# Kernel tuning notes

Hardware: AMD Instinct MI355X
Metric: run time of the kernel (lower is better)

## Reference

```python
import jax, jax.numpy as jnp
import numpy as np

N_NODES = 100000
N_EDGES = 3200000
HID = 16


def _graph_conv(x, src, dst, w_rel, w_root, b_rel, num_nodes):
    # PyG GraphConv: out_i = lin_rel(sum_{j in N(i)} x_j) + lin_root(x_i)
    agg = jax.ops.segment_sum(x[src], dst, num_segments=num_nodes)  # [N, d_in]
    return agg @ w_rel + b_rel + x @ w_root


def setup_inputs() -> dict:
    key = jax.random.key(0)
    ks = jax.random.split(key, 8)
    x = jax.random.normal(ks[0], (N_NODES, 1), dtype=jnp.float32)
    edge_index = jax.random.randint(ks[1], (2, N_EDGES), 0, N_NODES, dtype=jnp.int64)
    s = 1.0 / np.sqrt(HID)
    return {
        "x": x,
        "edge_index": edge_index,
        "enc_w_rel": jax.random.uniform(ks[2], (1, HID), jnp.float32, -1.0, 1.0),
        "enc_w_root": jax.random.uniform(ks[3], (1, HID), jnp.float32, -1.0, 1.0),
        "enc_b": jnp.zeros((HID,), jnp.float32),
        "proc_w_rel": jax.random.uniform(ks[4], (HID, HID), jnp.float32, -s, s),
        "proc_w_root": jax.random.uniform(ks[5], (HID, HID), jnp.float32, -s, s),
        "proc_b": jnp.zeros((HID,), jnp.float32),
        "dec_w_rel": jax.random.uniform(ks[6], (HID, 1), jnp.float32, -s, s),
        "dec_w_root": jax.random.uniform(ks[7], (HID, 1), jnp.float32, -s, s),
        "dec_b": jnp.zeros((1,), jnp.float32),
    }


def reference(x, edge_index, enc_w_rel, enc_w_root, enc_b,
              proc_w_rel, proc_w_root, proc_b,
              dec_w_rel, dec_w_root, dec_b):
    num_nodes = x.shape[0]
    src, dst = edge_index[0], edge_index[1]
    z = _graph_conv(x, src, dst, enc_w_rel, enc_w_root, enc_b, num_nodes)
    z = jax.nn.relu(z)
    z = _graph_conv(z, src, dst, proc_w_rel, proc_w_root, proc_b, num_nodes)
    y = _graph_conv(z, src, dst, dec_w_rel, dec_w_root, dec_b, num_nodes)
    return jax.nn.relu(y)
```

## Files before the change

kernel.cpp:

```cpp
#include <hip/hip_runtime.h>
#include <hip/hip_bf16.h>

#define HID 16
#define SB_BITS 11
#define SBLK (1 << SB_BITS)
#define SUBS 128
#define NBMAX 64
#define GSTRIDE 16
#define PT_THREADS 256
#define PT_K 16
#define PT_EDGES (PT_THREADS * PT_K)
#define ROWP 65

__global__ void k_init(int* __restrict__ p, int n) {
    int i = blockIdx.x * blockDim.x + threadIdx.x;
    if (i < n) p[i] = 0;
}

__global__ void k_passA(const int* __restrict__ src, const int* __restrict__ dst,
                        unsigned* __restrict__ bucketsA, int* __restrict__ gcurA,
                        int E, int nb, int capA) {
    __shared__ int cnt[NBMAX];
    __shared__ int pos[NBMAX];
    __shared__ int gbase[NBMAX];
    __shared__ unsigned reorder[PT_EDGES];
    __shared__ unsigned char bbk[PT_EDGES];
    int tb = blockIdx.x * PT_EDGES;
    int nE = min(PT_EDGES, E - tb);
    if (threadIdx.x < nb) cnt[threadIdx.x] = 0;
    __syncthreads();
    int kk[PT_K]; int rk[PT_K]; unsigned pk[PT_K];
#pragma unroll
    for (int k = 0; k < PT_K; k++) {
        int e = tb + k * PT_THREADS + threadIdx.x;
        if (e < E) {
            int s = src[e], d = dst[e];
            int b = d >> SB_BITS;
            kk[k] = b;
            pk[k] = ((unsigned)(d & (SBLK - 1)) << 17) | (unsigned)s;
            rk[k] = atomicAdd(&cnt[b], 1);
        } else kk[k] = -1;
    }
    __syncthreads();
    if (threadIdx.x == 0) {
        int acc = 0;
        for (int b = 0; b < nb; b++) { pos[b] = acc; acc += cnt[b]; }
    }
    __syncthreads();
    if (threadIdx.x < nb && cnt[threadIdx.x] > 0)
        gbase[threadIdx.x] = atomicAdd(&gcurA[threadIdx.x * GSTRIDE], cnt[threadIdx.x]);
    __syncthreads();
#pragma unroll
    for (int k = 0; k < PT_K; k++) {
        if (kk[k] >= 0) {
            int idx = pos[kk[k]] + rk[k];
            reorder[idx] = pk[k];
            bbk[idx] = (unsigned char)kk[k];
        }
    }
    __syncthreads();
    for (int idx = threadIdx.x; idx < nE; idx += PT_THREADS) {
        int b = bbk[idx];
        int g = gbase[b] + (idx - pos[b]);
        if (g < capA) bucketsA[(size_t)b * capA + g] = reorder[idx];
    }
}

__global__ void k_passB(const unsigned* __restrict__ bucketsA, const int* __restrict__ gcurA,
                        unsigned* __restrict__ bucketsB, int* __restrict__ gcurB,
                        int capA, int capSub, int tilesB) {
    int j = blockIdx.x / tilesB;
    int tile = blockIdx.x - j * tilesB;
    int cnt_j = min(gcurA[j * GSTRIDE], capA);
    int tb = tile * PT_EDGES;
    if (tb >= cnt_j) return;
    int nE = min(PT_EDGES, cnt_j - tb);
    __shared__ int cnt[SUBS];
    __shared__ int pos[SUBS];
    __shared__ int gb[SUBS];
    __shared__ unsigned reorder[PT_EDGES];
    __shared__ unsigned char bbk[PT_EDGES];
    if (threadIdx.x < SUBS) cnt[threadIdx.x] = 0;
    __syncthreads();
    const unsigned* in = bucketsA + (size_t)j * capA + tb;
    int kk[PT_K]; int rk[PT_K]; unsigned pk[PT_K];
#pragma unroll
    for (int k = 0; k < PT_K; k++) {
        int e = k * PT_THREADS + threadIdx.x;
        if (e < nE) {
            unsigned p = in[e];
            int dloc = (int)(p >> 17);
            int s = dloc >> 4;
            kk[k] = s;
            pk[k] = ((p & 0x1FFFFu) << 4) | (unsigned)(dloc & 15);
            rk[k] = atomicAdd(&cnt[s], 1);
        } else kk[k] = -1;
    }
    __syncthreads();
    if (threadIdx.x == 0) {
        int acc = 0;
        for (int s = 0; s < SUBS; s++) { pos[s] = acc; acc += cnt[s]; }
    }
    __syncthreads();
    if (threadIdx.x < SUBS && cnt[threadIdx.x] > 0)
        gb[threadIdx.x] = atomicAdd(&gcurB[j * SUBS + threadIdx.x], cnt[threadIdx.x]);
    __syncthreads();
#pragma unroll
    for (int k = 0; k < PT_K; k++) {
        if (kk[k] >= 0) {
            int idx = pos[kk[k]] + rk[k];
            reorder[idx] = pk[k];
            bbk[idx] = (unsigned char)kk[k];
        }
    }
    __syncthreads();
    for (int idx = threadIdx.x; idx < nE; idx += PT_THREADS) {
        int s = bbk[idx];
        int g = gb[s] + (idx - pos[s]);
        if (g < capSub) bucketsB[(size_t)(j * SUBS + s) * capSub + g] = reorder[idx];
    }
}

__global__ void __launch_bounds__(256)
k_agg1(const unsigned* __restrict__ bucketsB, const int* __restrict__ gcurB,
       const float* __restrict__ val, float* __restrict__ outD,
       int nq, int capSub, int N) {
    __shared__ float P[4 * 16 * ROWP];
    int wv = threadIdx.x >> 6, lane = threadIdx.x & 63;
    int q = blockIdx.x * 4 + wv;
    float* p = P + wv * 16 * ROWP;
#pragma unroll
    for (int d = 0; d < 16; d++) p[d * ROWP + lane] = 0.f;
    if (q < nq) {
        int cnt = min(gcurB[q], capSub);
        const unsigned* bk = bucketsB + (size_t)q * capSub;
        for (int e = lane; e < cnt; e += 64) {
            unsigned pk = bk[e];
            float v = val[pk >> 4];
            int a = (int)(pk & 15) * ROWP + lane;
            p[a] += v;
        }
    }
    __builtin_amdgcn_wave_barrier();
    int d = lane & 15, c0 = (lane >> 4) * 16;
    float s = 0.f;
#pragma unroll
    for (int k = 0; k < 16; k++) s += p[d * ROWP + c0 + k];
    s += __shfl_xor(s, 16);
    s += __shfl_xor(s, 32);
    if (q < nq && lane < 16) {
        int n = q * 16 + lane;
        if (n < N) outD[n] = s;
    }
}

__global__ void __launch_bounds__(256)
k_agg1f(const unsigned* __restrict__ bucketsB, const int* __restrict__ gcurB,
        const float* __restrict__ val, const float* __restrict__ R,
        float* __restrict__ out, int nq, int capSub, int N) {
    __shared__ float P[4 * 16 * ROWP];
    int wv = threadIdx.x >> 6, lane = threadIdx.x & 63;
    int q = blockIdx.x * 4 + wv;
    float* p = P + wv * 16 * ROWP;
#pragma unroll
    for (int d = 0; d < 16; d++) p[d * ROWP + lane] = 0.f;
    if (q < nq) {
        int cnt = min(gcurB[q], capSub);
        const unsigned* bk = bucketsB + (size_t)q * capSub;
        for (int e = lane; e < cnt; e += 64) {
            unsigned pk = bk[e];
            float v = val[pk >> 4];
            int a = (int)(pk & 15) * ROWP + lane;
            p[a] += v;
        }
    }
    __builtin_amdgcn_wave_barrier();
    int d = lane & 15, c0 = (lane >> 4) * 16;
    float s = 0.f;
#pragma unroll
    for (int k = 0; k < 16; k++) s += p[d * ROWP + c0 + k];
    s += __shfl_xor(s, 16);
    s += __shfl_xor(s, 32);
    if (q < nq && lane < 16) {
        int n = q * 16 + lane;
        if (n < N) out[n] = fmaxf(s + R[n], 0.f);
    }
}

__global__ void __launch_bounds__(256)
k_agg2(const unsigned* __restrict__ bucketsB, const int* __restrict__ gcurB,
       const float* __restrict__ val2, float* __restrict__ D2,
       int nq, int capSub, int N) {
    __shared__ float P[4 * 2 * 16 * ROWP];
    int wv = threadIdx.x >> 6, lane = threadIdx.x & 63;
    int q = blockIdx.x * 4 + wv;
    float* pa = P + wv * 2 * 16 * ROWP;
    float* pb = pa + 16 * ROWP;
#pragma unroll
    for (int d = 0; d < 16; d++) { pa[d * ROWP + lane] = 0.f; pb[d * ROWP + lane] = 0.f; }
    const float2* v2 = (const float2*)val2;
    if (q < nq) {
        int cnt = min(gcurB[q], capSub);
        const unsigned* bk = bucketsB + (size_t)q * capSub;
        for (int e = lane; e < cnt; e += 64) {
            unsigned pk = bk[e];
            float2 v = v2[pk >> 4];
            int a = (int)(pk & 15) * ROWP + lane;
            pa[a] += v.x;
            pb[a] += v.y;
        }
    }
    __builtin_amdgcn_wave_barrier();
    int d = lane & 15, c0 = (lane >> 4) * 16;
    float sa = 0.f, sb = 0.f;
#pragma unroll
    for (int k = 0; k < 16; k++) {
        sa += pa[d * ROWP + c0 + k];
        sb += pb[d * ROWP + c0 + k];
    }
    sa += __shfl_xor(sa, 16); sa += __shfl_xor(sa, 32);
    sb += __shfl_xor(sb, 16); sb += __shfl_xor(sb, 32);
    if (q < nq && lane < 16) {
        int n = q * 16 + lane;
        if (n < N) ((float2*)D2)[n] = make_float2(sa, sb);
    }
}

__global__ void k_encode(const float* __restrict__ x, const float* __restrict__ D1,
                         const float* __restrict__ ewrel, const float* __restrict__ ewroot,
                         const float* __restrict__ eb,
                         const float* __restrict__ pwrel, const float* __restrict__ pwroot,
                         const float* __restrict__ dwrel, const float* __restrict__ dwroot,
                         float* __restrict__ SAB, float* __restrict__ G1,
                         float* __restrict__ G2, int N) {
    __shared__ float su1[HID], su2[HID], sv1[HID], sv2[HID];
    __shared__ float swr[HID], swo[HID], sbb[HID];
    int t = threadIdx.x;
    if (t < 64) {
        int k = t & 15, w = t >> 4;
        const float* M  = (w < 2) ? pwrel : pwroot;
        const float* vv = ((w & 1) == 0) ? dwrel : dwroot;
        float acc = 0.f;
        for (int h = 0; h < HID; h++) acc += M[k * HID + h] * vv[h];
        if (w == 0) su1[k] = acc;
        else if (w == 1) su2[k] = acc;
        else if (w == 2) sv1[k] = acc;
        else sv2[k] = acc;
    }
    if (t < HID) { swr[t] = ewrel[t]; swo[t] = ewroot[t]; sbb[t] = eb[t]; }
    __syncthreads();
    int i = blockIdx.x * blockDim.x + t;
    if (i >= N) return;
    float a1 = D1[i], xi = x[i];
    float sa = 0.f, sb = 0.f, g1 = 0.f, g2 = 0.f;
#pragma unroll
    for (int h = 0; h < HID; h++) {
        float z = fmaxf(fmaf(a1, swr[h], fmaf(xi, swo[h], sbb[h])), 0.f);
        sa = fmaf(z, su1[h], sa);
        sb = fmaf(z, su2[h], sb);
        g1 = fmaf(z, sv1[h], g1);
        g2 = fmaf(z, sv2[h], g2);
    }
    SAB[2 * i] = sa; SAB[2 * i + 1] = sb; G1[i] = g1; G2[i] = g2;
}

__global__ void k_mid(const float* __restrict__ D2,
                      const float* __restrict__ G1, const float* __restrict__ G2,
                      const float* __restrict__ pb, const float* __restrict__ dwrel,
                      const float* __restrict__ dwroot, const float* __restrict__ db,
                      float* __restrict__ BETA, float* __restrict__ R, int N) {
    __shared__ float sc1, sc2, sbd;
    if (threadIdx.x == 0) {
        float c1 = 0.f, c2 = 0.f;
        for (int h = 0; h < HID; h++) { c1 += pb[h] * dwrel[h]; c2 += pb[h] * dwroot[h]; }
        sc1 = c1; sc2 = c2; sbd = db[0];
    }
    __syncthreads();
    int i = blockIdx.x * blockDim.x + threadIdx.x;
    if (i >= N) return;
    float2 d2 = ((const float2*)D2)[i];
    BETA[i] = d2.x + G1[i] + sc1;
    R[i]    = d2.y + G2[i] + sc2 + sbd;
}

extern "C" void kernel_launch(void* const* d_in, const int* in_sizes, int n_in,
                              void* d_out, int out_size, void* d_ws, size_t ws_size,
                              hipStream_t stream) {
    const float* x      = (const float*)d_in[0];
    const int*   ei     = (const int*)d_in[1];
    const float* ewrel  = (const float*)d_in[2];
    const float* ewroot = (const float*)d_in[3];
    const float* eb     = (const float*)d_in[4];
    const float* pwrel  = (const float*)d_in[5];
    const float* pwroot = (const float*)d_in[6];
    const float* pb     = (const float*)d_in[7];
    const float* dwrel  = (const float*)d_in[8];
    const float* dwroot = (const float*)d_in[9];
    const float* db     = (const float*)d_in[10];
    float* out = (float*)d_out;

    const int N = in_sizes[0];
    const int E = in_sizes[1] / 2;
    const int* src = ei;
    const int* dst = ei + E;

    const int nb = (N + SBLK - 1) >> SB_BITS;
    int capA = ((E / nb + 2048) + PT_EDGES - 1) & ~(PT_EDGES - 1);
    const int tilesB = capA / PT_EDGES;
    const int nq = nb * SUBS;
    int capSub = ((E / nq + 200) + 3) & ~3;

    size_t off = 0;
    int* gcurA = (int*)d_ws;                    off += NBMAX * GSTRIDE;
    int* gcurB = (int*)d_ws + off;              off += nq;
    off = (off + 255) & ~(size_t)255;
    unsigned* bucketsA = (unsigned*)d_ws + off; off += (size_t)nb * capA;
    unsigned* bucketsB = (unsigned*)d_ws + off; off += (size_t)nq * capSub;
    float* SAB  = (float*)d_ws + off;           off += (size_t)2 * N;
    float* G1   = (float*)d_ws + off;           off += N;
    float* G2   = (float*)d_ws + off;           off += N;
    float* BETA = (float*)d_ws + off;           off += N;
    float* R    = (float*)d_ws + off;           off += N;
    float* D1   = (float*)d_ws + off;           off += N;
    float* D2   = (float*)d_ws + off;           off += (size_t)2 * N;

    const int zeroWords = NBMAX * GSTRIDE + nq;
    const int ntilesA = (E + PT_EDGES - 1) / PT_EDGES;
    const int nodeBlocks = (N + 255) / 256;
    const int aggBlocks = (nq + 3) / 4;

    hipLaunchKernelGGL(k_init, dim3((zeroWords + 255) / 256), dim3(256), 0, stream,
                       gcurA, zeroWords);
    hipLaunchKernelGGL(k_passA, dim3(ntilesA), dim3(PT_THREADS), 0, stream,
                       src, dst, bucketsA, gcurA, E, nb, capA);
    hipLaunchKernelGGL(k_passB, dim3(nb * tilesB), dim3(PT_THREADS), 0, stream,
                       bucketsA, gcurA, bucketsB, gcurB, capA, capSub, tilesB);

    hipLaunchKernelGGL(k_agg1, dim3(aggBlocks), dim3(256), 0, stream,
                       bucketsB, gcurB, x, D1, nq, capSub, N);
    hipLaunchKernelGGL(k_encode, dim3(nodeBlocks), dim3(256), 0, stream,
                       x, D1, ewrel, ewroot, eb, pwrel, pwroot,
                       dwrel, dwroot, SAB, G1, G2, N);

    hipLaunchKernelGGL(k_agg2, dim3(aggBlocks), dim3(256), 0, stream,
                       bucketsB, gcurB, SAB, D2, nq, capSub, N);
    hipLaunchKernelGGL(k_mid, dim3(nodeBlocks), dim3(256), 0, stream,
                       D2, G1, G2, pb, dwrel, dwroot, db, BETA, R, N);

    hipLaunchKernelGGL(k_agg1f, dim3(aggBlocks), dim3(256), 0, stream,
                       bucketsB, gcurB, BETA, R, out, nq, capSub, N);
}
```

Baseline: 184.9 us.

## Replace atomic shared-memory binning with per-thread counters, split sort into three passes, fuse node kernels

```diff
diff --git a/kernel.cpp b/kernel.cpp
--- a/kernel.cpp
+++ b/kernel.cpp
@@ -3,236 +3,167 @@
 
 #define HID 16
 #define SB_BITS 11
-#define SBLK (1 << SB_BITS)
-#define SUBS 128
-#define NBMAX 64
+#define SBLK 2048
+#define NBA_MAX 52
+#define CSTRIDE 257
+#define PT 256
+#define PT_K 16
+#define PT_EDGES (PT * PT_K)
+#define ROWP 65
 #define GSTRIDE 16
-#define PT_THREADS 256
-#define PT_K 16
-#define PT_EDGES (PT_THREADS * PT_K)
-#define ROWP 65
 
 __global__ void k_init(int* __restrict__ p, int n) {
     int i = blockIdx.x * blockDim.x + threadIdx.x;
     if (i < n) p[i] = 0;
 }
 
-__global__ void k_passA(const int* __restrict__ src, const int* __restrict__ dst,
-                        unsigned* __restrict__ bucketsA, int* __restrict__ gcurA,
-                        int E, int nb, int capA) {
-    __shared__ int cnt[NBMAX];
-    __shared__ int pos[NBMAX];
-    __shared__ int gbase[NBMAX];
+__global__ void __launch_bounds__(PT)
+k_sortA(const int* __restrict__ src, const int* __restrict__ dst,
+        unsigned* __restrict__ outb, int* __restrict__ gcurA,
+        int E, int nb, int capA) {
+    __shared__ int cntP[NBA_MAX * CSTRIDE];
+    __shared__ int chunkTot[NBA_MAX * 4];
+    __shared__ int binTot[NBA_MAX];
+    __shared__ int pos[NBA_MAX];
+    __shared__ int gbase[NBA_MAX];
     __shared__ unsigned reorder[PT_EDGES];
     __shared__ unsigned char bbk[PT_EDGES];
+    int tid = threadIdx.x, w = tid >> 6, l = tid & 63;
     int tb = blockIdx.x * PT_EDGES;
     int nE = min(PT_EDGES, E - tb);
-    if (threadIdx.x < nb) cnt[threadIdx.x] = 0;
-    __syncthreads();
-    int kk[PT_K]; int rk[PT_K]; unsigned pk[PT_K];
+    for (int b = 0; b < nb; b++) cntP[b * CSTRIDE + tid] = 0;
+    __syncthreads();
+    unsigned pk[PT_K]; int rr[PT_K]; int rk[PT_K];
 #pragma unroll
     for (int k = 0; k < PT_K; k++) {
-        int e = tb + k * PT_THREADS + threadIdx.x;
+        int e = tb + k * PT + tid;
+        rr[k] = -1;
         if (e < E) {
             int s = src[e], d = dst[e];
             int b = d >> SB_BITS;
-            kk[k] = b;
+            rr[k] = b;
             pk[k] = ((unsigned)(d & (SBLK - 1)) << 17) | (unsigned)s;
-            rk[k] = atomicAdd(&cnt[b], 1);
-        } else kk[k] = -1;
-    }
-    __syncthreads();
-    if (threadIdx.x == 0) {
+            int idx = b * CSTRIDE + tid;
+            int o = cntP[idx]; cntP[idx] = o + 1; rk[k] = o;
+        }
+    }
+    __syncthreads();
+    if (l < nb) {
+        int acc = 0, base = l * CSTRIDE + (w << 6);
+        for (int t = 0; t < 64; t++) { int v = cntP[base + t]; cntP[base + t] = acc; acc += v; }
+        chunkTot[l * 4 + w] = acc;
+    }
+    __syncthreads();
+    if (tid < nb) {
         int acc = 0;
-        for (int b = 0; b < nb; b++) { pos[b] = acc; acc += cnt[b]; }
-    }
-    __syncthreads();
-    if (threadIdx.x < nb && cnt[threadIdx.x] > 0)
-        gbase[threadIdx.x] = atomicAdd(&gcurA[threadIdx.x * GSTRIDE], cnt[threadIdx.x]);
+        for (int ww = 0; ww < 4; ww++) { int v = chunkTot[tid * 4 + ww]; chunkTot[tid * 4 + ww] = acc; acc += v; }
+        binTot[tid] = acc;
+    }
+    __syncthreads();
+    if (tid == 0) { int acc = 0; for (int b = 0; b < nb; b++) { pos[b] = acc; acc += binTot[b]; } }
+    __syncthreads();
+    if (tid < nb && binTot[tid] > 0)
+        gbase[tid] = atomicAdd(&gcurA[tid * GSTRIDE], binTot[tid]);
     __syncthreads();
 #pragma unroll
     for (int k = 0; k < PT_K; k++) {
-        if (kk[k] >= 0) {
-            int idx = pos[kk[k]] + rk[k];
+        if (rr[k] >= 0) {
+            int b = rr[k];
+            int idx = pos[b] + chunkTot[b * 4 + w] + cntP[b * CSTRIDE + tid] + rk[k];
             reorder[idx] = pk[k];
-            bbk[idx] = (unsigned char)kk[k];
-        }
-    }
-    __syncthreads();
-    for (int idx = threadIdx.x; idx < nE; idx += PT_THREADS) {
+            bbk[idx] = (unsigned char)b;
+        }
+    }
+    __syncthreads();
+    for (int idx = tid; idx < nE; idx += PT) {
         int b = bbk[idx];
         int g = gbase[b] + (idx - pos[b]);
-        if (g < capA) bucketsA[(size_t)b * capA + g] = reorder[idx];
-    }
-}
-
-__global__ void k_passB(const unsigned* __restrict__ bucketsA, const int* __restrict__ gcurA,
-                        unsigned* __restrict__ bucketsB, int* __restrict__ gcurB,
-                        int capA, int capSub, int tilesB) {
-    int j = blockIdx.x / tilesB;
-    int tile = blockIdx.x - j * tilesB;
-    int cnt_j = min(gcurA[j * GSTRIDE], capA);
+        if (g < capA) outb[(size_t)b * capA + g] = reorder[idx];
+    }
+}
+
+template<int NB, int PASS>
+__global__ void __launch_bounds__(PT)
+k_sortB(const unsigned* __restrict__ inb, const int* __restrict__ incur, int inCurStride,
+        unsigned* __restrict__ outb, int* __restrict__ outcur,
+        int capIn, int capOut, int tilesPerRow) {
+    int row = blockIdx.x / tilesPerRow;
+    int tile = blockIdx.x - row * tilesPerRow;
+    int cnt_row = min(incur[row * inCurStride], capIn);
     int tb = tile * PT_EDGES;
-    if (tb >= cnt_j) return;
-    int nE = min(PT_EDGES, cnt_j - tb);
-    __shared__ int cnt[SUBS];
-    __shared__ int pos[SUBS];
-    __shared__ int gb[SUBS];
+    if (tb >= cnt_row) return;
+    int nE = min(PT_EDGES, cnt_row - tb);
+    __shared__ int cntP[NB * CSTRIDE];
+    __shared__ int chunkTot[NB * 4];
+    __shared__ int binTot[NB];
+    __shared__ int pos[NB];
+    __shared__ int gbase[NB];
     __shared__ unsigned reorder[PT_EDGES];
     __shared__ unsigned char bbk[PT_EDGES];
-    if (threadIdx.x < SUBS) cnt[threadIdx.x] = 0;
-    __syncthreads();
-    const unsigned* in = bucketsA + (size_t)j * capA + tb;
-    int kk[PT_K]; int rk[PT_K]; unsigned pk[PT_K];
+    int tid = threadIdx.x, w = tid >> 6, l = tid & 63;
+    for (int b = 0; b < NB; b++) cntP[b * CSTRIDE + tid] = 0;
+    __syncthreads();
+    const unsigned* in = inb + (size_t)row * capIn + tb;
+    unsigned pk[PT_K]; int rr[PT_K]; int rk[PT_K];
 #pragma unroll
     for (int k = 0; k < PT_K; k++) {
-        int e = k * PT_THREADS + threadIdx.x;
+        int e = k * PT + tid;
+        rr[k] = -1;
         if (e < nE) {
             unsigned p = in[e];
-            int dloc = (int)(p >> 17);
-            int s = dloc >> 4;
-            kk[k] = s;
-            pk[k] = ((p & 0x1FFFFu) << 4) | (unsigned)(dloc & 15);
-            rk[k] = atomicAdd(&cnt[s], 1);
-        } else kk[k] = -1;
-    }
-    __syncthreads();
-    if (threadIdx.x == 0) {
+            int b = (PASS == 1) ? (int)(p >> 24) : (int)(p >> 21);
+            rr[k] = b;
+            pk[k] = (PASS == 1) ? (p & 0x00FFFFFFu)
+                                : (((p & 0x1FFFFu) << 4) | ((p >> 17) & 15u));
+            int idx = b * CSTRIDE + tid;
+            int o = cntP[idx]; cntP[idx] = o + 1; rk[k] = o;
+        }
+    }
+    __syncthreads();
+    if (l < NB) {
+        int acc = 0, base = l * CSTRIDE + (w << 6);
+        for (int t = 0; t < 64; t++) { int v = cntP[base + t]; cntP[base + t] = acc; acc += v; }
+        chunkTot[l * 4 + w] = acc;
+    }
+    __syncthreads();
+    if (tid < NB) {
         int acc = 0;
-        for (int s = 0; s < SUBS; s++) { pos[s] = acc; acc += cnt[s]; }
-    }
-    __syncthreads();
-    if (threadIdx.x < SUBS && cnt[threadIdx.x] > 0)
-        gb[threadIdx.x] = atomicAdd(&gcurB[j * SUBS + threadIdx.x], cnt[threadIdx.x]);
+        for (int ww = 0; ww < 4; ww++) { int v = chunkTot[tid * 4 + ww]; chunkTot[tid * 4 + ww] = acc; acc += v; }
+        binTot[tid] = acc;
+    }
+    __syncthreads();
+    if (tid == 0) { int acc = 0; for (int b = 0; b < NB; b++) { pos[b] = acc; acc += binTot[b]; } }
+    __syncthreads();
+    if (tid < NB && binTot[tid] > 0)
+        gbase[tid] = atomicAdd(&outcur[row * NB + tid], binTot[tid]);
     __syncthreads();
 #pragma unroll
     for (int k = 0; k < PT_K; k++) {
-        if (kk[k] >= 0) {
-            int idx = pos[kk[k]] + rk[k];
+        if (rr[k] >= 0) {
+            int b = rr[k];
+            int idx = pos[b] + chunkTot[b * 4 + w] + cntP[b * CSTRIDE + tid] + rk[k];
             reorder[idx] = pk[k];
-            bbk[idx] = (unsigned char)kk[k];
-        }
-    }
-    __syncthreads();
-    for (int idx = threadIdx.x; idx < nE; idx += PT_THREADS) {
-        int s = bbk[idx];
-        int g = gb[s] + (idx - pos[s]);
-        if (g < capSub) bucketsB[(size_t)(j * SUBS + s) * capSub + g] = reorder[idx];
+            bbk[idx] = (unsigned char)b;
+        }
+    }
+    __syncthreads();
+    for (int idx = tid; idx < nE; idx += PT) {
+        int b = bbk[idx];
+        int g = gbase[b] + (idx - pos[b]);
+        if (g < capOut) outb[(size_t)(row * NB + b) * capOut + g] = reorder[idx];
     }
 }
 
 __global__ void __launch_bounds__(256)
-k_agg1(const unsigned* __restrict__ bucketsB, const int* __restrict__ gcurB,
-       const float* __restrict__ val, float* __restrict__ outD,
-       int nq, int capSub, int N) {
+k_agg1enc(const unsigned* __restrict__ bk2, const int* __restrict__ gcurB2,
+          const float* __restrict__ x,
+          const float* __restrict__ ewrel, const float* __restrict__ ewroot,
+          const float* __restrict__ eb,
+          const float* __restrict__ pwrel, const float* __restrict__ pwroot,
+          const float* __restrict__ dwrel, const float* __restrict__ dwroot,
+          float* __restrict__ SAB, float* __restrict__ G1, float* __restrict__ G2,
+          int capSub, int N) {
     __shared__ float P[4 * 16 * ROWP];
-    int wv = threadIdx.x >> 6, lane = threadIdx.x & 63;
-    int q = blockIdx.x * 4 + wv;
-    float* p = P + wv * 16 * ROWP;
-#pragma unroll
-    for (int d = 0; d < 16; d++) p[d * ROWP + lane] = 0.f;
-    if (q < nq) {
-        int cnt = min(gcurB[q], capSub);
-        const unsigned* bk = bucketsB + (size_t)q * capSub;
-        for (int e = lane; e < cnt; e += 64) {
-            unsigned pk = bk[e];
-            float v = val[pk >> 4];
-            int a = (int)(pk & 15) * ROWP + lane;
-            p[a] += v;
-        }
-    }
-    __builtin_amdgcn_wave_barrier();
-    int d = lane & 15, c0 = (lane >> 4) * 16;
-    float s = 0.f;
-#pragma unroll
-    for (int k = 0; k < 16; k++) s += p[d * ROWP + c0 + k];
-    s += __shfl_xor(s, 16);
-    s += __shfl_xor(s, 32);
-    if (q < nq && lane < 16) {
-        int n = q * 16 + lane;
-        if (n < N) outD[n] = s;
-    }
-}
-
-__global__ void __launch_bounds__(256)
-k_agg1f(const unsigned* __restrict__ bucketsB, const int* __restrict__ gcurB,
-        const float* __restrict__ val, const float* __restrict__ R,
-        float* __restrict__ out, int nq, int capSub, int N) {
-    __shared__ float P[4 * 16 * ROWP];
-    int wv = threadIdx.x >> 6, lane = threadIdx.x & 63;
-    int q = blockIdx.x * 4 + wv;
-    float* p = P + wv * 16 * ROWP;
-#pragma unroll
-    for (int d = 0; d < 16; d++) p[d * ROWP + lane] = 0.f;
-    if (q < nq) {
-        int cnt = min(gcurB[q], capSub);
-        const unsigned* bk = bucketsB + (size_t)q * capSub;
-        for (int e = lane; e < cnt; e += 64) {
-            unsigned pk = bk[e];
-            float v = val[pk >> 4];
-            int a = (int)(pk & 15) * ROWP + lane;
-            p[a] += v;
-        }
-    }
-    __builtin_amdgcn_wave_barrier();
-    int d = lane & 15, c0 = (lane >> 4) * 16;
-    float s = 0.f;
-#pragma unroll
-    for (int k = 0; k < 16; k++) s += p[d * ROWP + c0 + k];
-    s += __shfl_xor(s, 16);
-    s += __shfl_xor(s, 32);
-    if (q < nq && lane < 16) {
-        int n = q * 16 + lane;
-        if (n < N) out[n] = fmaxf(s + R[n], 0.f);
-    }
-}
-
-__global__ void __launch_bounds__(256)
-k_agg2(const unsigned* __restrict__ bucketsB, const int* __restrict__ gcurB,
-       const float* __restrict__ val2, float* __restrict__ D2,
-       int nq, int capSub, int N) {
-    __shared__ float P[4 * 2 * 16 * ROWP];
-    int wv = threadIdx.x >> 6, lane = threadIdx.x & 63;
-    int q = blockIdx.x * 4 + wv;
-    float* pa = P + wv * 2 * 16 * ROWP;
-    float* pb = pa + 16 * ROWP;
-#pragma unroll
-    for (int d = 0; d < 16; d++) { pa[d * ROWP + lane] = 0.f; pb[d * ROWP + lane] = 0.f; }
-    const float2* v2 = (const float2*)val2;
-    if (q < nq) {
-        int cnt = min(gcurB[q], capSub);
-        const unsigned* bk = bucketsB + (size_t)q * capSub;
-        for (int e = lane; e < cnt; e += 64) {
-            unsigned pk = bk[e];
-            float2 v = v2[pk >> 4];
-            int a = (int)(pk & 15) * ROWP + lane;
-            pa[a] += v.x;
-            pb[a] += v.y;
-        }
-    }
-    __builtin_amdgcn_wave_barrier();
-    int d = lane & 15, c0 = (lane >> 4) * 16;
-    float sa = 0.f, sb = 0.f;
-#pragma unroll
-    for (int k = 0; k < 16; k++) {
-        sa += pa[d * ROWP + c0 + k];
-        sb += pb[d * ROWP + c0 + k];
-    }
-    sa += __shfl_xor(sa, 16); sa += __shfl_xor(sa, 32);
-    sb += __shfl_xor(sb, 16); sb += __shfl_xor(sb, 32);
-    if (q < nq && lane < 16) {
-        int n = q * 16 + lane;
-        if (n < N) ((float2*)D2)[n] = make_float2(sa, sb);
-    }
-}
-
-__global__ void k_encode(const float* __restrict__ x, const float* __restrict__ D1,
-                         const float* __restrict__ ewrel, const float* __restrict__ ewroot,
-                         const float* __restrict__ eb,
-                         const float* __restrict__ pwrel, const float* __restrict__ pwroot,
-                         const float* __restrict__ dwrel, const float* __restrict__ dwroot,
-                         float* __restrict__ SAB, float* __restrict__ G1,
-                         float* __restrict__ G2, int N) {
     __shared__ float su1[HID], su2[HID], sv1[HID], sv2[HID];
     __shared__ float swr[HID], swo[HID], sbb[HID];
     int t = threadIdx.x;
@@ -248,39 +179,139 @@
         else sv2[k] = acc;
     }
     if (t < HID) { swr[t] = ewrel[t]; swo[t] = ewroot[t]; sbb[t] = eb[t]; }
-    __syncthreads();
-    int i = blockIdx.x * blockDim.x + t;
-    if (i >= N) return;
-    float a1 = D1[i], xi = x[i];
-    float sa = 0.f, sb = 0.f, g1 = 0.f, g2 = 0.f;
-#pragma unroll
-    for (int h = 0; h < HID; h++) {
-        float z = fmaxf(fmaf(a1, swr[h], fmaf(xi, swo[h], sbb[h])), 0.f);
-        sa = fmaf(z, su1[h], sa);
-        sb = fmaf(z, su2[h], sb);
-        g1 = fmaf(z, sv1[h], g1);
-        g2 = fmaf(z, sv2[h], g2);
-    }
-    SAB[2 * i] = sa; SAB[2 * i + 1] = sb; G1[i] = g1; G2[i] = g2;
-}
-
-__global__ void k_mid(const float* __restrict__ D2,
-                      const float* __restrict__ G1, const float* __restrict__ G2,
-                      const float* __restrict__ pb, const float* __restrict__ dwrel,
-                      const float* __restrict__ dwroot, const float* __restrict__ db,
-                      float* __restrict__ BETA, float* __restrict__ R, int N) {
+    int wv = t >> 6, lane = t & 63;
+    int q = blockIdx.x * 4 + wv;
+    float* p = P + wv * 16 * ROWP;
+#pragma unroll
+    for (int d = 0; d < 16; d++) p[d * ROWP + lane] = 0.f;
+    __syncthreads();
+    int cnt = min(gcurB2[q], capSub);
+    const unsigned* bk = bk2 + (size_t)q * capSub;
+    int e = lane;
+    for (; e + 64 < cnt; e += 128) {
+        unsigned pk0 = bk[e], pk1 = bk[e + 64];
+        float v0 = x[pk0 >> 4], v1 = x[pk1 >> 4];
+        p[(int)(pk0 & 15) * ROWP + lane] += v0;
+        p[(int)(pk1 & 15) * ROWP + lane] += v1;
+    }
+    if (e < cnt) { unsigned pk = bk[e]; p[(int)(pk & 15) * ROWP + lane] += x[pk >> 4]; }
+    __builtin_amdgcn_wave_barrier();
+    int d = lane & 15, c0 = (lane >> 4) * 16;
+    float s = 0.f;
+#pragma unroll
+    for (int k = 0; k < 16; k++) s += p[d * ROWP + c0 + k];
+    s += __shfl_xor(s, 16);
+    s += __shfl_xor(s, 32);
+    if (lane < 16) {
+        int n = q * 16 + lane;
+        if (n < N) {
+            float a1 = s, xi = x[n];
+            float sa = 0.f, sb = 0.f, g1 = 0.f, g2 = 0.f;
+#pragma unroll
+            for (int h = 0; h < HID; h++) {
+                float z = fmaxf(fmaf(a1, swr[h], fmaf(xi, swo[h], sbb[h])), 0.f);
+                sa = fmaf(z, su1[h], sa);
+                sb = fmaf(z, su2[h], sb);
+                g1 = fmaf(z, sv1[h], g1);
+                g2 = fmaf(z, sv2[h], g2);
+            }
+            ((float2*)SAB)[n] = make_float2(sa, sb);
+            G1[n] = g1; G2[n] = g2;
+        }
+    }
+}
+
+__global__ void __launch_bounds__(256)
+k_agg2mid(const unsigned* __restrict__ bk2, const int* __restrict__ gcurB2,
+          const float* __restrict__ SAB,
+          const float* __restrict__ G1, const float* __restrict__ G2,
+          const float* __restrict__ pb, const float* __restrict__ dwrel,
+          const float* __restrict__ dwroot, const float* __restrict__ db,
+          float* __restrict__ BETA, float* __restrict__ R,
+          int capSub, int N) {
+    __shared__ float P[4 * 2 * 16 * ROWP];
     __shared__ float sc1, sc2, sbd;
-    if (threadIdx.x == 0) {
+    int t = threadIdx.x;
+    if (t == 0) {
         float c1 = 0.f, c2 = 0.f;
         for (int h = 0; h < HID; h++) { c1 += pb[h] * dwrel[h]; c2 += pb[h] * dwroot[h]; }
         sc1 = c1; sc2 = c2; sbd = db[0];
     }
-    __syncthreads();
-    int i = blockIdx.x * blockDim.x + threadIdx.x;
-    if (i >= N) return;
-    float2 d2 = ((const float2*)D2)[i];
-    BETA[i] = d2.x + G1[i] + sc1;
-    R[i]    = d2.y + G2[i] + sc2 + sbd;
+    int wv = t >> 6, lane = t & 63;
+    int q = blockIdx.x * 4 + wv;
+    float* pa = P + wv * 2 * 16 * ROWP;
+    float* pbn = pa + 16 * ROWP;
+#pragma unroll
+    for (int d = 0; d < 16; d++) { pa[d * ROWP + lane] = 0.f; pbn[d * ROWP + lane] = 0.f; }
+    __syncthreads();
+    int cnt = min(gcurB2[q], capSub);
+    const unsigned* bk = bk2 + (size_t)q * capSub;
+    const float2* v2 = (const float2*)SAB;
+    int e = lane;
+    for (; e + 64 < cnt; e += 128) {
+        unsigned pk0 = bk[e], pk1 = bk[e + 64];
+        float2 v0 = v2[pk0 >> 4], v1 = v2[pk1 >> 4];
+        int a0 = (int)(pk0 & 15) * ROWP + lane;
+        int a1 = (int)(pk1 & 15) * ROWP + lane;
+        pa[a0] += v0.x; pbn[a0] += v0.y;
+        pa[a1] += v1.x; pbn[a1] += v1.y;
+    }
+    if (e < cnt) {
+        unsigned pk = bk[e];
+        float2 v = v2[pk >> 4];
+        int a = (int)(pk & 15) * ROWP + lane;
+        pa[a] += v.x; pbn[a] += v.y;
+    }
+    __builtin_amdgcn_wave_barrier();
+    int d = lane & 15, c0 = (lane >> 4) * 16;
+    float sa = 0.f, sb = 0.f;
+#pragma unroll
+    for (int k = 0; k < 16; k++) {
+        sa += pa[d * ROWP + c0 + k];
+        sb += pbn[d * ROWP + c0 + k];
+    }
+    sa += __shfl_xor(sa, 16); sa += __shfl_xor(sa, 32);
+    sb += __shfl_xor(sb, 16); sb += __shfl_xor(sb, 32);
+    if (lane < 16) {
+        int n = q * 16 + lane;
+        if (n < N) {
+            BETA[n] = sa + G1[n] + sc1;
+            R[n]    = sb + G2[n] + sc2 + sbd;
+        }
+    }
+}
+
+__global__ void __launch_bounds__(256)
+k_agg1f(const unsigned* __restrict__ bk2, const int* __restrict__ gcurB2,
+        const float* __restrict__ val, const float* __restrict__ R,
+        float* __restrict__ out, int capSub, int N) {
+    __shared__ float P[4 * 16 * ROWP];
+    int wv = threadIdx.x >> 6, lane = threadIdx.x & 63;
+    int q = blockIdx.x * 4 + wv;
+    float* p = P + wv * 16 * ROWP;
+#pragma unroll
+    for (int d = 0; d < 16; d++) p[d * ROWP + lane] = 0.f;
+    int cnt = min(gcurB2[q], capSub);
+    const unsigned* bk = bk2 + (size_t)q * capSub;
+    int e = lane;
+    for (; e + 64 < cnt; e += 128) {
+        unsigned pk0 = bk[e], pk1 = bk[e + 64];
+        float v0 = val[pk0 >> 4], v1 = val[pk1 >> 4];
+        p[(int)(pk0 & 15) * ROWP + lane] += v0;
+        p[(int)(pk1 & 15) * ROWP + lane] += v1;
+    }
+    if (e < cnt) { unsigned pk = bk[e]; p[(int)(pk & 15) * ROWP + lane] += val[pk >> 4]; }
+    __builtin_amdgcn_wave_barrier();
+    int d = lane & 15, c0 = (lane >> 4) * 16;
+    float s = 0.f;
+#pragma unroll
+    for (int k = 0; k < 16; k++) s += p[d * ROWP + c0 + k];
+    s += __shfl_xor(s, 16);
+    s += __shfl_xor(s, 32);
+    if (lane < 16) {
+        int n = q * 16 + lane;
+        if (n < N) out[n] = fmaxf(s + R[n], 0.f);
+    }
 }
 
 extern "C" void kernel_launch(void* const* d_in, const int* in_sizes, int n_in,
@@ -304,49 +335,48 @@
     const int* src = ei;
     const int* dst = ei + E;
 
-    const int nb = (N + SBLK - 1) >> SB_BITS;
-    int capA = ((E / nb + 2048) + PT_EDGES - 1) & ~(PT_EDGES - 1);
-    const int tilesB = capA / PT_EDGES;
-    const int nq = nb * SUBS;
-    int capSub = ((E / nq + 200) + 3) & ~3;
+    const int nbA = (N + SBLK - 1) >> SB_BITS;
+    int capA = ((E / nbA + 2048) + PT_EDGES - 1) & ~(PT_EDGES - 1);
+    const int tilesB1 = capA / PT_EDGES;
+    const int nRow1 = nbA * 16;
+    int capB1 = ((E / nRow1 + 640) + 3) & ~3;
+    const int tilesB2 = (capB1 + PT_EDGES - 1) / PT_EDGES;
+    const int nq = nbA * 128;
+    int capSub = ((E / nq + 226) + 3) & ~3;
 
     size_t off = 0;
-    int* gcurA = (int*)d_ws;                    off += NBMAX * GSTRIDE;
-    int* gcurB = (int*)d_ws + off;              off += nq;
+    int* gcurA  = (int*)d_ws;                  off += (size_t)nbA * GSTRIDE;
+    int* gcurB1 = (int*)d_ws + off;            off += nRow1;
+    int* gcurB2 = (int*)d_ws + off;            off += nq;
+    const int zeroWords = (int)off;
     off = (off + 255) & ~(size_t)255;
-    unsigned* bucketsA = (unsigned*)d_ws + off; off += (size_t)nb * capA;
-    unsigned* bucketsB = (unsigned*)d_ws + off; off += (size_t)nq * capSub;
-    float* SAB  = (float*)d_ws + off;           off += (size_t)2 * N;
-    float* G1   = (float*)d_ws + off;           off += N;
-    float* G2   = (float*)d_ws + off;           off += N;
-    float* BETA = (float*)d_ws + off;           off += N;
-    float* R    = (float*)d_ws + off;           off += N;
-    float* D1   = (float*)d_ws + off;           off += N;
-    float* D2   = (float*)d_ws + off;           off += (size_t)2 * N;
-
-    const int zeroWords = NBMAX * GSTRIDE + nq;
+    unsigned* bucketsA  = (unsigned*)d_ws + off; off += (size_t)nbA * capA;
+    unsigned* bucketsB1 = (unsigned*)d_ws + off; off += (size_t)nRow1 * capB1;
+    unsigned* bucketsB2 = (unsigned*)d_ws + off; off += (size_t)nq * capSub;
+    float* SAB  = (float*)d_ws + off;          off += (size_t)2 * N;
+    float* G1   = (float*)d_ws + off;          off += N;
+    float* G2   = (float*)d_ws + off;          off += N;
+    float* BETA = (float*)d_ws + off;          off += N;
+    float* R    = (float*)d_ws + off;          off += N;
+
     const int ntilesA = (E + PT_EDGES - 1) / PT_EDGES;
-    const int nodeBlocks = (N + 255) / 256;
-    const int aggBlocks = (nq + 3) / 4;
+    const int aggBlocks = nq / 4;
 
     hipLaunchKernelGGL(k_init, dim3((zeroWords + 255) / 256), dim3(256), 0, stream,
                        gcurA, zeroWords);
-    hipLaunchKernelGGL(k_passA, dim3(ntilesA), dim3(PT_THREADS), 0, stream,
-                       src, dst, bucketsA, gcurA, E, nb, capA);
-    hipLaunchKernelGGL(k_passB, dim3(nb * tilesB), dim3(PT_THREADS), 0, stream,
-                       bucketsA, gcurA, bucketsB, gcurB, capA, capSub, tilesB);
-
-    hipLaunchKernelGGL(k_agg1, dim3(aggBlocks), dim3(256), 0, stream,
-                       bucketsB, gcurB, x, D1, nq, capSub, N);
-    hipLaunchKernelGGL(k_encode, dim3(nodeBlocks), dim3(256), 0, stream,
-                       x, D1, ewrel, ewroot, eb, pwrel, pwroot,
-                       dwrel, dwroot, SAB, G1, G2, N);
-
-    hipLaunchKernelGGL(k_agg2, dim3(aggBlocks), dim3(256), 0, stream,
-                       bucketsB, gcurB, SAB, D2, nq, capSub, N);
-    hipLaunchKernelGGL(k_mid, dim3(nodeBlocks), dim3(256), 0, stream,
-                       D2, G1, G2, pb, dwrel, dwroot, db, BETA, R, N);
-
+    hipLaunchKernelGGL(k_sortA, dim3(ntilesA), dim3(PT), 0, stream,
+                       src, dst, bucketsA, gcurA, E, nbA, capA);
+    hipLaunchKernelGGL((k_sortB<16, 1>), dim3(nbA * tilesB1), dim3(PT), 0, stream,
+                       bucketsA, gcurA, GSTRIDE, bucketsB1, gcurB1, capA, capB1, tilesB1);
+    hipLaunchKernelGGL((k_sortB<8, 2>), dim3(nRow1 * tilesB2), dim3(PT), 0, stream,
+                       bucketsB1, gcurB1, 1, bucketsB2, gcurB2, capB1, capSub, tilesB2);
+
+    hipLaunchKernelGGL(k_agg1enc, dim3(aggBlocks), dim3(256), 0, stream,
+                       bucketsB2, gcurB2, x, ewrel, ewroot, eb, pwrel, pwroot,
+                       dwrel, dwroot, SAB, G1, G2, capSub, N);
+    hipLaunchKernelGGL(k_agg2mid, dim3(aggBlocks), dim3(256), 0, stream,
+                       bucketsB2, gcurB2, SAB, G1, G2, pb, dwrel, dwroot, db,
+                       BETA, R, capSub, N);
     hipLaunchKernelGGL(k_agg1f, dim3(aggBlocks), dim3(256), 0, stream,
-                       bucketsB, gcurB, BETA, R, out, nq, capSub, N);
-}
+                       bucketsB2, gcurB2, BETA, R, out, capSub, N);
+}
```

Result: slower. 218.6 us (+18.2%).
